# Optimization experiments

Hardware: AMD Instinct MI355X
Metric: run time of the kernel (lower is better)

The kernel has to match this reference:

```python
import jax, jax.numpy as jnp
import numpy as np

N, E = 50000, 800000
IN_DIM, HID, H, L = 256, 128, 4, 2
HD = HID // H
EPS = 1e-5


def _bn(x, g, b):
    # training-mode BatchNorm1d: biased variance over batch dim, eps=1e-5
    m = x.mean(0)
    v = jnp.var(x, axis=0)
    return g * (x - m) * jax.lax.rsqrt(v + EPS) + b


def _seg_softmax(scores, dst, n):
    # scores: [E, H]; softmax over edges sharing the same dst node
    m = jax.ops.segment_max(scores, dst, num_segments=n)  # [N, H]
    e = jnp.exp(scores - m[dst])
    s = jax.ops.segment_sum(e, dst, num_segments=n)
    return e / s[dst]


def _attn_layer(h, src, dst, wq, bq, wk, bk, wv, bv, wo, bo):
    n = h.shape[0]
    scale = 1.0 / np.sqrt(HD)
    Q = (h @ wq + bq).reshape(n, H, HD)
    K = (h @ wk + bk).reshape(n, H, HD)
    V = (h @ wv + bv).reshape(n, H, HD)
    # per-edge scores: Q of src dotted with K of dst
    scores = jnp.einsum('ehd,ehd->eh', Q[src], K[dst]) * scale  # [E, H]
    attn = _seg_softmax(scores, dst, n)                         # [E, H]
    # weighted scatter-sum of V gathered at dst (faithful to source)
    out = jax.ops.segment_sum(attn[:, :, None] * V[dst], dst, num_segments=n)
    out = out.reshape(n, HID) @ wo + bo
    return jax.nn.relu(out)


def setup_inputs() -> dict:
    key = jax.random.key(0)
    ks = jax.random.split(key, 20)
    s = 0.05  # weight scale to keep activations tame
    inp = {
        'x': jax.random.normal(ks[0], (N, IN_DIM), jnp.float32),
        'edge_index': jax.random.randint(ks[1], (2, E), 0, N),
        'W_enc1': jax.random.normal(ks[2], (IN_DIM, HID), jnp.float32) * s,
        'b_enc1': jax.random.normal(ks[3], (HID,), jnp.float32) * s,
        'g1': jnp.ones((HID,), jnp.float32),
        'beta1': jnp.zeros((HID,), jnp.float32),
        'W_enc2': jax.random.normal(ks[4], (HID, HID), jnp.float32) * s,
        'b_enc2': jax.random.normal(ks[5], (HID,), jnp.float32) * s,
        'g2': jnp.ones((HID,), jnp.float32),
        'beta2': jnp.zeros((HID,), jnp.float32),
        'Wq': jax.random.normal(ks[6], (L, HID, HID), jnp.float32) * s,
        'bq': jax.random.normal(ks[7], (L, HID), jnp.float32) * s,
        'Wk': jax.random.normal(ks[8], (L, HID, HID), jnp.float32) * s,
        'bk': jax.random.normal(ks[9], (L, HID), jnp.float32) * s,
        'Wv': jax.random.normal(ks[10], (L, HID, HID), jnp.float32) * s,
        'bv': jax.random.normal(ks[11], (L, HID), jnp.float32) * s,
        'Wo': jax.random.normal(ks[12], (L, HID, HID), jnp.float32) * s,
        'bo': jax.random.normal(ks[13], (L, HID), jnp.float32) * s,
    }
    return inp


def reference(x, edge_index, W_enc1, b_enc1, g1, beta1, W_enc2, b_enc2, g2, beta2,
              Wq, bq, Wk, bk, Wv, bv, Wo, bo):
    src, dst = edge_index[0], edge_index[1]
    # encoder: Linear -> BN -> ReLU -> (dropout=id) -> Linear -> BN -> ReLU
    h = jax.nn.relu(_bn(x @ W_enc1 + b_enc1, g1, beta1))
    h = jax.nn.relu(_bn(h @ W_enc2 + b_enc2, g2, beta2))
    for i in range(L):
        h = _attn_layer(h, src, dst, Wq[i], bq[i], Wk[i], bk[i],
                        Wv[i], bv[i], Wo[i], bo[i])
    return h
```

## Files before the change

kernel.cpp:

```cpp
#include <hip/hip_runtime.h>

#define NN 50000
#define NE 800000
#define NB 782
#define TOTF 114688

typedef unsigned short u16;
typedef unsigned int u32;
typedef __attribute__((ext_vector_type(8))) short s8v;
typedef __attribute__((ext_vector_type(4))) float f4v;

__device__ __forceinline__ void split2(float f, u16& h, u16& lo) {
    u32 u = __float_as_uint(f);
    h = (u16)(u >> 16);
    float r = f - __uint_as_float(u & 0xFFFF0000u);
    lo = (u16)(__float_as_uint(r) >> 16);
}

__global__ void mask_scatter_k(const int* __restrict__ dst, float* __restrict__ mask) {
    int i = blockIdx.x * blockDim.x + threadIdx.x;
    if (i < NE) mask[dst[i]] = 1.0f;
}

__global__ void prep_w_k(const float* __restrict__ W1, const float* __restrict__ W2,
                         const float* __restrict__ Wv, const float* __restrict__ Wo,
                         u16* __restrict__ fh, u16* __restrict__ fl) {
    int idx = blockIdx.x * 256 + threadIdx.x;
    if (idx >= TOTF) return;
    const float* W;
    int local;
    if (idx < 32768) { W = W1; local = idx; }
    else {
        int t = idx - 32768;
        int m = t >> 14;
        local = t & 16383;
        if (m == 0) W = W2;
        else if (m == 1) W = Wv;
        else if (m == 2) W = Wo;
        else if (m == 3) W = Wv + 16384;
        else W = Wo + 16384;
    }
    int j = local & 7, l = (local >> 3) & 63, nt = (local >> 9) & 7, kc = local >> 12;
    int k = kc * 32 + ((l >> 4) << 3) + j;
    int n = nt * 16 + (l & 15);
    u16 h, lo;
    split2(W[k * 128 + n], h, lo);
    fh[idx] = h;
    fl[idx] = lo;
}

__global__ __launch_bounds__(64)
void redstats_k(const float* __restrict__ pst, float* __restrict__ st) {
    int c = blockIdx.x;
    float s = 0.f;
    for (int b = threadIdx.x; b < NB; b += 64) s += pst[(size_t)b * 256 + c];
    s += __shfl_xor(s, 1);  s += __shfl_xor(s, 2);  s += __shfl_xor(s, 4);
    s += __shfl_xor(s, 8);  s += __shfl_xor(s, 16); s += __shfl_xor(s, 32);
    if (threadIdx.x == 0) st[c] = s;
}

template<int KC, int FOLD, int STATS>
__global__ __launch_bounds__(512, 6)
void mgemm_k(const float* __restrict__ A,
             const u16* __restrict__ fh, const u16* __restrict__ fl,
             const float* __restrict__ bias,
             const float* __restrict__ fst,
             const float* __restrict__ fg, const float* __restrict__ fbe,
             float* __restrict__ pst,
             float* __restrict__ C) {
    constexpr int KP = KC / 4;
    __shared__ __align__(16) u16 Ah[64][136];
    __shared__ __align__(16) u16 Al[64][136];
    __shared__ float scl[128], shf[128];
    const int tid = threadIdx.x;
    const int l = tid & 63, w = tid >> 6;
    const int q = l >> 4, cc = l & 15;
    const int sl = w >> 1, hf = w & 1;
    const int row0 = blockIdx.x * 64;

    if (FOLD && tid < 128) {
        float mean = fst[tid] * (1.0f / NN);
        float var = fst[128 + tid] * (1.0f / NN) - mean * mean;
        float rstd = rsqrtf(var + 1e-5f);
        float ga = fg[tid] * rstd;
        scl[tid] = ga;
        shf[tid] = fbe[tid] - mean * ga;
    }

    f4v zf = {0.f, 0.f, 0.f, 0.f};
    f4v acc[4];
#pragma unroll
    for (int t = 0; t < 4; ++t) acc[t] = zf;

    for (int p = 0; p < KP; ++p) {
        if (p > 0 || FOLD) __syncthreads();
#pragma unroll
        for (int it = 0; it < 4; ++it) {
            int lin = tid + 512 * it;
            int r = lin >> 5;
            int c4 = (lin & 31) * 4;
            int gr = row0 + r; if (gr > NN - 1) gr = NN - 1;
            float4 f = *(const float4*)(A + (size_t)gr * (KC * 32) + p * 128 + c4);
            float v[4] = {f.x, f.y, f.z, f.w};
            if (FOLD) {
#pragma unroll
                for (int m = 0; m < 4; ++m) {
                    float t = v[m] * scl[c4 + m] + shf[c4 + m];
                    v[m] = t > 0.f ? t : 0.f;
                }
            }
            ushort4 uh, ul;
            split2(v[0], uh.x, ul.x); split2(v[1], uh.y, ul.y);
            split2(v[2], uh.z, ul.z); split2(v[3], uh.w, ul.w);
            *(ushort4*)&Ah[r][c4] = uh;
            *(ushort4*)&Al[r][c4] = ul;
        }
        __syncthreads();
#pragma unroll
        for (int kc = 0; kc < 4; ++kc) {
            int kcg = p * 4 + kc;
            s8v ah = *(const s8v*)&Ah[16 * sl + cc][kc * 32 + q * 8];
            s8v al = *(const s8v*)&Al[16 * sl + cc][kc * 32 + q * 8];
#pragma unroll
            for (int t = 0; t < 4; ++t) {
                const int fo = kcg * 4096 + (4 * hf + t) * 512 + l * 8;
                s8v bh = *(const s8v*)(fh + fo);
                s8v bl = *(const s8v*)(fl + fo);
                acc[t] = __builtin_amdgcn_mfma_f32_16x16x32_bf16(ah, bh, acc[t], 0, 0, 0);
                acc[t] = __builtin_amdgcn_mfma_f32_16x16x32_bf16(ah, bl, acc[t], 0, 0, 0);
                acc[t] = __builtin_amdgcn_mfma_f32_16x16x32_bf16(al, bh, acc[t], 0, 0, 0);
            }
        }
    }

    float ps[4], pq[4];
#pragma unroll
    for (int t = 0; t < 4; ++t) { ps[t] = 0.f; pq[t] = 0.f; }
#pragma unroll
    for (int t = 0; t < 4; ++t) {
        int col = (4 * hf + t) * 16 + cc;
        float bb = bias[col];
#pragma unroll
        for (int r = 0; r < 4; ++r) {
            int gr = row0 + 16 * sl + q * 4 + r;
            float val = acc[t][r] + bb;
            if (gr < NN) {
                C[(size_t)gr * 128 + col] = val;
                if (STATS) { ps[t] += val; pq[t] += val * val; }
            }
        }
    }
    if (STATS) {
        __syncthreads();
        float* wredS = (float*)&Ah[0][0];
        float* wredQ = wredS + 512;
#pragma unroll
        for (int t = 0; t < 4; ++t) {
            ps[t] += __shfl_xor(ps[t], 16); ps[t] += __shfl_xor(ps[t], 32);
            pq[t] += __shfl_xor(pq[t], 16); pq[t] += __shfl_xor(pq[t], 32);
        }
        if (l < 16) {
#pragma unroll
            for (int t = 0; t < 4; ++t) {
                int col = (4 * hf + t) * 16 + l;
                wredS[sl * 128 + col] = ps[t];
                wredQ[sl * 128 + col] = pq[t];
            }
        }
        __syncthreads();
        if (tid < 256) {
            int c = tid & 127;
            const float* src = (tid < 128) ? wredS : wredQ;
            pst[(size_t)blockIdx.x * 256 + tid] =
                src[c] + src[128 + c] + src[256 + c] + src[384 + c];
        }
    }
}

__global__ __launch_bounds__(512, 6)
void mmega_k(const float* __restrict__ X,
             const u16* __restrict__ fh, const u16* __restrict__ fl,
             const float* __restrict__ bv, const float* __restrict__ bo,
             const float* __restrict__ fst,
             const float* __restrict__ fg, const float* __restrict__ fbe,
             const float* __restrict__ mask, float* __restrict__ out) {
    __shared__ __align__(16) u16 Ah[64][136];
    __shared__ __align__(16) u16 Al[64][136];
    __shared__ float scl[128], shf[128];
    const int tid = threadIdx.x;
    const int l = tid & 63, w = tid >> 6;
    const int q = l >> 4, cc = l & 15;
    const int sl = w >> 1, hf = w & 1;
    const int row0 = blockIdx.x * 64;

    if (tid < 128) {
        float mean = fst[tid] * (1.0f / NN);
        float var = fst[128 + tid] * (1.0f / NN) - mean * mean;
        float rstd = rsqrtf(var + 1e-5f);
        float ga = fg[tid] * rstd;
        scl[tid] = ga;
        shf[tid] = fbe[tid] - mean * ga;
    }
    __syncthreads();

    float rm[4];
#pragma unroll
    for (int r = 0; r < 4; ++r) {
        int gr = row0 + 16 * sl + q * 4 + r;
        rm[r] = (gr < NN) ? mask[gr] : 0.f;
    }

#pragma unroll
    for (int it = 0; it < 4; ++it) {
        int lin = tid + 512 * it;
        int r = lin >> 5;
        int c4 = (lin & 31) * 4;
        int gr = row0 + r; if (gr > NN - 1) gr = NN - 1;
        float4 f = *(const float4*)(X + (size_t)gr * 128 + c4);
        float v[4] = {f.x, f.y, f.z, f.w};
        ushort4 uh, ul;
#pragma unroll
        for (int m = 0; m < 4; ++m) {
            float t = v[m] * scl[c4 + m] + shf[c4 + m];
            v[m] = t > 0.f ? t : 0.f;
        }
        split2(v[0], uh.x, ul.x); split2(v[1], uh.y, ul.y);
        split2(v[2], uh.z, ul.z); split2(v[3], uh.w, ul.w);
        *(ushort4*)&Ah[r][c4] = uh;
        *(ushort4*)&Al[r][c4] = ul;
    }
    __syncthreads();

    f4v zf = {0.f, 0.f, 0.f, 0.f};
    for (int s = 0; s < 4; ++s) {
        const u16* WH = fh + s * 16384;
        const u16* WL = fl + s * 16384;
        const float* bp = (s == 0) ? bv : (s == 1) ? bo : (s == 2) ? (bv + 128) : (bo + 128);

        f4v acc[4];
#pragma unroll
        for (int t = 0; t < 4; ++t) acc[t] = zf;
#pragma unroll
        for (int kc = 0; kc < 4; ++kc) {
            s8v ah = *(const s8v*)&Ah[16 * sl + cc][kc * 32 + q * 8];
            s8v al = *(const s8v*)&Al[16 * sl + cc][kc * 32 + q * 8];
#pragma unroll
            for (int t = 0; t < 4; ++t) {
                const int fo = kc * 4096 + (4 * hf + t) * 512 + l * 8;
                s8v bh = *(const s8v*)(WH + fo);
                s8v bl = *(const s8v*)(WL + fo);
                acc[t] = __builtin_amdgcn_mfma_f32_16x16x32_bf16(ah, bh, acc[t], 0, 0, 0);
                acc[t] = __builtin_amdgcn_mfma_f32_16x16x32_bf16(ah, bl, acc[t], 0, 0, 0);
                acc[t] = __builtin_amdgcn_mfma_f32_16x16x32_bf16(al, bh, acc[t], 0, 0, 0);
            }
        }

        if (s == 3) {
#pragma unroll
            for (int t = 0; t < 4; ++t) {
                int col = (4 * hf + t) * 16 + cc;
                float bb = bp[col];
#pragma unroll
                for (int r = 0; r < 4; ++r) {
                    int gr = row0 + 16 * sl + q * 4 + r;
                    if (gr < NN)
                        out[(size_t)gr * 128 + col] = fmaxf(acc[t][r] + bb, 0.f);
                }
            }
        } else {
            __syncthreads();
#pragma unroll
            for (int t = 0; t < 4; ++t) {
                int col = (4 * hf + t) * 16 + cc;
                float bb = bp[col];
#pragma unroll
                for (int r = 0; r < 4; ++r) {
                    int rl = 16 * sl + q * 4 + r;
                    float val = acc[t][r] + bb;
                    val = (s == 1) ? fmaxf(val, 0.f) : val * rm[r];
                    u16 h, lo; split2(val, h, lo);
                    Ah[rl][col] = h;
                    Al[rl][col] = lo;
                }
            }
            __syncthreads();
        }
    }
}

extern "C" void kernel_launch(void* const* d_in, const int* in_sizes, int n_in,
                              void* d_out, int out_size, void* d_ws, size_t ws_size,
                              hipStream_t stream) {
    const float* x   = (const float*)d_in[0];
    const int*   ei  = (const int*)d_in[1];
    const float* W1  = (const float*)d_in[2];
    const float* b1  = (const float*)d_in[3];
    const float* g1  = (const float*)d_in[4];
    const float* be1 = (const float*)d_in[5];
    const float* W2  = (const float*)d_in[6];
    const float* b2  = (const float*)d_in[7];
    const float* g2  = (const float*)d_in[8];
    const float* be2 = (const float*)d_in[9];
    const float* Wv  = (const float*)d_in[14];
    const float* bv  = (const float*)d_in[15];
    const float* Wo  = (const float*)d_in[16];
    const float* bo  = (const float*)d_in[17];

    float* out = (float*)d_out;

    char* ws = (char*)d_ws;
    float* buf  = (float*)(ws);
    float* mask = (float*)(ws + 25600000);
    float* st1  = (float*)(ws + 25800704);
    float* st2  = st1 + 256;
    u16*   fH   = (u16*)(ws + 25804800);
    u16*   fL   = fH + TOTF;
    float* pst  = (float*)(ws + 26263552);

    hipMemsetAsync(mask, 0, NN * sizeof(float), stream);
    mask_scatter_k<<<dim3((NE + 255) / 256), dim3(256), 0, stream>>>(ei + NE, mask);
    prep_w_k<<<dim3((TOTF + 255) / 256), dim3(256), 0, stream>>>(W1, W2, Wv, Wo, fH, fL);

    dim3 gg(NB), bb(512);
    mgemm_k<8, 0, 1><<<gg, bb, 0, stream>>>(x, fH, fL, b1,
                                            nullptr, nullptr, nullptr, pst, buf);
    redstats_k<<<dim3(256), dim3(64), 0, stream>>>(pst, st1);
    mgemm_k<4, 1, 1><<<gg, bb, 0, stream>>>(buf, fH + 32768, fL + 32768, b2,
                                            st1, g1, be1, pst, out);
    redstats_k<<<dim3(256), dim3(64), 0, stream>>>(pst, st2);
    mmega_k<<<gg, bb, 0, stream>>>(out, fH + 49152, fL + 49152, bv, bo,
                                   st2, g2, be2, mask, out);
}
```

Baseline: 227.3 us.

## Give each wave a private 32-row by 128-column tile to drop block barriers

The GEMM kernels switch from 512-thread blocks over 64 rows to 256-thread blocks over 128 rows. Each wave now owns 32 full rows: it stages them into LDS, computes all eight column tiles with two row-tile accumulators, and in the chained mmega kernel writes its intermediate results back only to its own rows. Because no wave reads another wave's rows, most __syncthreads calls go away, and each weight fragment loaded from global memory feeds twice as many MFMAs. In exchange each thread holds more accumulator registers (launch bounds drop to 2 blocks per CU), the grid halves to 391 blocks, which can leave the CUs unevenly loaded, and every wave has to load its own rows with less parallelism per row.

```diff
diff --git a/kernel.cpp b/kernel.cpp
--- a/kernel.cpp
+++ b/kernel.cpp
@@ -2,7 +2,7 @@
 
 #define NN 50000
 #define NE 800000
-#define NB 782
+#define NB 391
 #define TOTF 114688
 
 typedef unsigned short u16;
@@ -60,7 +60,7 @@
 }
 
 template<int KC, int FOLD, int STATS>
-__global__ __launch_bounds__(512, 6)
+__global__ __launch_bounds__(256, 2)
 void mgemm_k(const float* __restrict__ A,
              const u16* __restrict__ fh, const u16* __restrict__ fl,
              const float* __restrict__ bias,
@@ -68,39 +68,41 @@
              const float* __restrict__ fg, const float* __restrict__ fbe,
              float* __restrict__ pst,
              float* __restrict__ C) {
+    constexpr int K = KC * 32;
     constexpr int KP = KC / 4;
-    __shared__ __align__(16) u16 Ah[64][136];
-    __shared__ __align__(16) u16 Al[64][136];
+    __shared__ __align__(16) u16 Ah[128][136];
+    __shared__ __align__(16) u16 Al[128][136];
     __shared__ float scl[128], shf[128];
     const int tid = threadIdx.x;
     const int l = tid & 63, w = tid >> 6;
     const int q = l >> 4, cc = l & 15;
-    const int sl = w >> 1, hf = w & 1;
-    const int row0 = blockIdx.x * 64;
-
-    if (FOLD && tid < 128) {
-        float mean = fst[tid] * (1.0f / NN);
-        float var = fst[128 + tid] * (1.0f / NN) - mean * mean;
-        float rstd = rsqrtf(var + 1e-5f);
-        float ga = fg[tid] * rstd;
-        scl[tid] = ga;
-        shf[tid] = fbe[tid] - mean * ga;
+    const int row0 = blockIdx.x * 128;
+
+    if (FOLD) {
+        if (tid < 128) {
+            float mean = fst[tid] * (1.0f / NN);
+            float var = fst[128 + tid] * (1.0f / NN) - mean * mean;
+            float rstd = rsqrtf(var + 1e-5f);
+            float ga = fg[tid] * rstd;
+            scl[tid] = ga;
+            shf[tid] = fbe[tid] - mean * ga;
+        }
+        __syncthreads();
     }
 
     f4v zf = {0.f, 0.f, 0.f, 0.f};
-    f4v acc[4];
-#pragma unroll
-    for (int t = 0; t < 4; ++t) acc[t] = zf;
+    f4v acc0[8], acc1[8];
+#pragma unroll
+    for (int nt = 0; nt < 8; ++nt) { acc0[nt] = zf; acc1[nt] = zf; }
 
     for (int p = 0; p < KP; ++p) {
-        if (p > 0 || FOLD) __syncthreads();
-#pragma unroll
-        for (int it = 0; it < 4; ++it) {
-            int lin = tid + 512 * it;
+#pragma unroll
+        for (int it = 0; it < 16; ++it) {
+            int lin = it * 64 + l;
             int r = lin >> 5;
             int c4 = (lin & 31) * 4;
-            int gr = row0 + r; if (gr > NN - 1) gr = NN - 1;
-            float4 f = *(const float4*)(A + (size_t)gr * (KC * 32) + p * 128 + c4);
+            int gr = row0 + 32 * w + r; if (gr > NN - 1) gr = NN - 1;
+            float4 f = *(const float4*)(A + (size_t)gr * K + p * 128 + c4);
             float v[4] = {f.x, f.y, f.z, f.w};
             if (FOLD) {
 #pragma unroll
@@ -112,41 +114,48 @@
             ushort4 uh, ul;
             split2(v[0], uh.x, ul.x); split2(v[1], uh.y, ul.y);
             split2(v[2], uh.z, ul.z); split2(v[3], uh.w, ul.w);
-            *(ushort4*)&Ah[r][c4] = uh;
-            *(ushort4*)&Al[r][c4] = ul;
-        }
-        __syncthreads();
+            *(ushort4*)&Ah[32 * w + r][c4] = uh;
+            *(ushort4*)&Al[32 * w + r][c4] = ul;
+        }
 #pragma unroll
         for (int kc = 0; kc < 4; ++kc) {
             int kcg = p * 4 + kc;
-            s8v ah = *(const s8v*)&Ah[16 * sl + cc][kc * 32 + q * 8];
-            s8v al = *(const s8v*)&Al[16 * sl + cc][kc * 32 + q * 8];
-#pragma unroll
-            for (int t = 0; t < 4; ++t) {
-                const int fo = kcg * 4096 + (4 * hf + t) * 512 + l * 8;
+            s8v ah0 = *(const s8v*)&Ah[32 * w + cc][kc * 32 + q * 8];
+            s8v al0 = *(const s8v*)&Al[32 * w + cc][kc * 32 + q * 8];
+            s8v ah1 = *(const s8v*)&Ah[32 * w + 16 + cc][kc * 32 + q * 8];
+            s8v al1 = *(const s8v*)&Al[32 * w + 16 + cc][kc * 32 + q * 8];
+#pragma unroll
+            for (int nt = 0; nt < 8; ++nt) {
+                const int fo = kcg * 4096 + nt * 512 + l * 8;
                 s8v bh = *(const s8v*)(fh + fo);
                 s8v bl = *(const s8v*)(fl + fo);
-                acc[t] = __builtin_amdgcn_mfma_f32_16x16x32_bf16(ah, bh, acc[t], 0, 0, 0);
-                acc[t] = __builtin_amdgcn_mfma_f32_16x16x32_bf16(ah, bl, acc[t], 0, 0, 0);
-                acc[t] = __builtin_amdgcn_mfma_f32_16x16x32_bf16(al, bh, acc[t], 0, 0, 0);
-            }
-        }
-    }
-
-    float ps[4], pq[4];
-#pragma unroll
-    for (int t = 0; t < 4; ++t) { ps[t] = 0.f; pq[t] = 0.f; }
-#pragma unroll
-    for (int t = 0; t < 4; ++t) {
-        int col = (4 * hf + t) * 16 + cc;
+                acc0[nt] = __builtin_amdgcn_mfma_f32_16x16x32_bf16(ah0, bh, acc0[nt], 0, 0, 0);
+                acc0[nt] = __builtin_amdgcn_mfma_f32_16x16x32_bf16(ah0, bl, acc0[nt], 0, 0, 0);
+                acc0[nt] = __builtin_amdgcn_mfma_f32_16x16x32_bf16(al0, bh, acc0[nt], 0, 0, 0);
+                acc1[nt] = __builtin_amdgcn_mfma_f32_16x16x32_bf16(ah1, bh, acc1[nt], 0, 0, 0);
+                acc1[nt] = __builtin_amdgcn_mfma_f32_16x16x32_bf16(ah1, bl, acc1[nt], 0, 0, 0);
+                acc1[nt] = __builtin_amdgcn_mfma_f32_16x16x32_bf16(al1, bh, acc1[nt], 0, 0, 0);
+            }
+        }
+    }
+
+    float ps[8], pq[8];
+#pragma unroll
+    for (int nt = 0; nt < 8; ++nt) { ps[nt] = 0.f; pq[nt] = 0.f; }
+#pragma unroll
+    for (int nt = 0; nt < 8; ++nt) {
+        int col = nt * 16 + cc;
         float bb = bias[col];
 #pragma unroll
-        for (int r = 0; r < 4; ++r) {
-            int gr = row0 + 16 * sl + q * 4 + r;
-            float val = acc[t][r] + bb;
-            if (gr < NN) {
-                C[(size_t)gr * 128 + col] = val;
-                if (STATS) { ps[t] += val; pq[t] += val * val; }
+        for (int rt = 0; rt < 2; ++rt) {
+#pragma unroll
+            for (int r = 0; r < 4; ++r) {
+                int gr = row0 + 32 * w + 16 * rt + q * 4 + r;
+                float val = (rt ? acc1[nt][r] : acc0[nt][r]) + bb;
+                if (gr < NN) {
+                    C[(size_t)gr * 128 + col] = val;
+                    if (STATS) { ps[nt] += val; pq[nt] += val * val; }
+                }
             }
         }
     }
@@ -155,20 +164,19 @@
         float* wredS = (float*)&Ah[0][0];
         float* wredQ = wredS + 512;
 #pragma unroll
-        for (int t = 0; t < 4; ++t) {
-            ps[t] += __shfl_xor(ps[t], 16); ps[t] += __shfl_xor(ps[t], 32);
-            pq[t] += __shfl_xor(pq[t], 16); pq[t] += __shfl_xor(pq[t], 32);
+        for (int nt = 0; nt < 8; ++nt) {
+            ps[nt] += __shfl_xor(ps[nt], 16); ps[nt] += __shfl_xor(ps[nt], 32);
+            pq[nt] += __shfl_xor(pq[nt], 16); pq[nt] += __shfl_xor(pq[nt], 32);
         }
         if (l < 16) {
 #pragma unroll
-            for (int t = 0; t < 4; ++t) {
-                int col = (4 * hf + t) * 16 + l;
-                wredS[sl * 128 + col] = ps[t];
-                wredQ[sl * 128 + col] = pq[t];
+            for (int nt = 0; nt < 8; ++nt) {
+                wredS[w * 128 + nt * 16 + l] = ps[nt];
+                wredQ[w * 128 + nt * 16 + l] = pq[nt];
             }
         }
         __syncthreads();
-        if (tid < 256) {
+        {
             int c = tid & 127;
             const float* src = (tid < 128) ? wredS : wredQ;
             pst[(size_t)blockIdx.x * 256 + tid] =
@@ -177,21 +185,20 @@
     }
 }
 
-__global__ __launch_bounds__(512, 6)
+__global__ __launch_bounds__(256, 2)
 void mmega_k(const float* __restrict__ X,
              const u16* __restrict__ fh, const u16* __restrict__ fl,
              const float* __restrict__ bv, const float* __restrict__ bo,
              const float* __restrict__ fst,
              const float* __restrict__ fg, const float* __restrict__ fbe,
              const float* __restrict__ mask, float* __restrict__ out) {
-    __shared__ __align__(16) u16 Ah[64][136];
-    __shared__ __align__(16) u16 Al[64][136];
+    __shared__ __align__(16) u16 Ah[128][136];
+    __shared__ __align__(16) u16 Al[128][136];
     __shared__ float scl[128], shf[128];
     const int tid = threadIdx.x;
     const int l = tid & 63, w = tid >> 6;
     const int q = l >> 4, cc = l & 15;
-    const int sl = w >> 1, hf = w & 1;
-    const int row0 = blockIdx.x * 64;
+    const int row0 = blockIdx.x * 128;
 
     if (tid < 128) {
         float mean = fst[tid] * (1.0f / NN);
@@ -203,33 +210,34 @@
     }
     __syncthreads();
 
-    float rm[4];
-#pragma unroll
-    for (int r = 0; r < 4; ++r) {
-        int gr = row0 + 16 * sl + q * 4 + r;
-        rm[r] = (gr < NN) ? mask[gr] : 0.f;
-    }
-
-#pragma unroll
-    for (int it = 0; it < 4; ++it) {
-        int lin = tid + 512 * it;
+    float rm[2][4];
+#pragma unroll
+    for (int rt = 0; rt < 2; ++rt)
+#pragma unroll
+        for (int r = 0; r < 4; ++r) {
+            int gr = row0 + 32 * w + 16 * rt + q * 4 + r;
+            rm[rt][r] = (gr < NN) ? mask[gr] : 0.f;
+        }
+
+#pragma unroll
+    for (int it = 0; it < 16; ++it) {
+        int lin = it * 64 + l;
         int r = lin >> 5;
         int c4 = (lin & 31) * 4;
-        int gr = row0 + r; if (gr > NN - 1) gr = NN - 1;
+        int gr = row0 + 32 * w + r; if (gr > NN - 1) gr = NN - 1;
         float4 f = *(const float4*)(X + (size_t)gr * 128 + c4);
         float v[4] = {f.x, f.y, f.z, f.w};
-        ushort4 uh, ul;
 #pragma unroll
         for (int m = 0; m < 4; ++m) {
             float t = v[m] * scl[c4 + m] + shf[c4 + m];
             v[m] = t > 0.f ? t : 0.f;
         }
+        ushort4 uh, ul;
         split2(v[0], uh.x, ul.x); split2(v[1], uh.y, ul.y);
         split2(v[2], uh.z, ul.z); split2(v[3], uh.w, ul.w);
-        *(ushort4*)&Ah[r][c4] = uh;
-        *(ushort4*)&Al[r][c4] = ul;
-    }
-    __syncthreads();
+        *(ushort4*)&Ah[32 * w + r][c4] = uh;
+        *(ushort4*)&Al[32 * w + r][c4] = ul;
+    }
 
     f4v zf = {0.f, 0.f, 0.f, 0.f};
     for (int s = 0; s < 4; ++s) {
@@ -237,53 +245,61 @@
         const u16* WL = fl + s * 16384;
         const float* bp = (s == 0) ? bv : (s == 1) ? bo : (s == 2) ? (bv + 128) : (bo + 128);
 
-        f4v acc[4];
-#pragma unroll
-        for (int t = 0; t < 4; ++t) acc[t] = zf;
+        f4v acc0[8], acc1[8];
+#pragma unroll
+        for (int nt = 0; nt < 8; ++nt) { acc0[nt] = zf; acc1[nt] = zf; }
 #pragma unroll
         for (int kc = 0; kc < 4; ++kc) {
-            s8v ah = *(const s8v*)&Ah[16 * sl + cc][kc * 32 + q * 8];
-            s8v al = *(const s8v*)&Al[16 * sl + cc][kc * 32 + q * 8];
-#pragma unroll
-            for (int t = 0; t < 4; ++t) {
-                const int fo = kc * 4096 + (4 * hf + t) * 512 + l * 8;
+            s8v ah0 = *(const s8v*)&Ah[32 * w + cc][kc * 32 + q * 8];
+            s8v al0 = *(const s8v*)&Al[32 * w + cc][kc * 32 + q * 8];
+            s8v ah1 = *(const s8v*)&Ah[32 * w + 16 + cc][kc * 32 + q * 8];
+            s8v al1 = *(const s8v*)&Al[32 * w + 16 + cc][kc * 32 + q * 8];
+#pragma unroll
+            for (int nt = 0; nt < 8; ++nt) {
+                const int fo = kc * 4096 + nt * 512 + l * 8;
                 s8v bh = *(const s8v*)(WH + fo);
                 s8v bl = *(const s8v*)(WL + fo);
-                acc[t] = __builtin_amdgcn_mfma_f32_16x16x32_bf16(ah, bh, acc[t], 0, 0, 0);
-                acc[t] = __builtin_amdgcn_mfma_f32_16x16x32_bf16(ah, bl, acc[t], 0, 0, 0);
-                acc[t] = __builtin_amdgcn_mfma_f32_16x16x32_bf16(al, bh, acc[t], 0, 0, 0);
+                acc0[nt] = __builtin_amdgcn_mfma_f32_16x16x32_bf16(ah0, bh, acc0[nt], 0, 0, 0);
+                acc0[nt] = __builtin_amdgcn_mfma_f32_16x16x32_bf16(ah0, bl, acc0[nt], 0, 0, 0);
+                acc0[nt] = __builtin_amdgcn_mfma_f32_16x16x32_bf16(al0, bh, acc0[nt], 0, 0, 0);
+                acc1[nt] = __builtin_amdgcn_mfma_f32_16x16x32_bf16(ah1, bh, acc1[nt], 0, 0, 0);
+                acc1[nt] = __builtin_amdgcn_mfma_f32_16x16x32_bf16(ah1, bl, acc1[nt], 0, 0, 0);
+                acc1[nt] = __builtin_amdgcn_mfma_f32_16x16x32_bf16(al1, bh, acc1[nt], 0, 0, 0);
             }
         }
 
         if (s == 3) {
 #pragma unroll
-            for (int t = 0; t < 4; ++t) {
-                int col = (4 * hf + t) * 16 + cc;
+            for (int nt = 0; nt < 8; ++nt) {
+                int col = nt * 16 + cc;
                 float bb = bp[col];
 #pragma unroll
-                for (int r = 0; r < 4; ++r) {
-                    int gr = row0 + 16 * sl + q * 4 + r;
-                    if (gr < NN)
-                        out[(size_t)gr * 128 + col] = fmaxf(acc[t][r] + bb, 0.f);
-                }
+                for (int rt = 0; rt < 2; ++rt)
+#pragma unroll
+                    for (int r = 0; r < 4; ++r) {
+                        int gr = row0 + 32 * w + 16 * rt + q * 4 + r;
+                        if (gr < NN)
+                            out[(size_t)gr * 128 + col] =
+                                fmaxf((rt ? acc1[nt][r] : acc0[nt][r]) + bb, 0.f);
+                    }
             }
         } else {
-            __syncthreads();
-#pragma unroll
-            for (int t = 0; t < 4; ++t) {
-                int col = (4 * hf + t) * 16 + cc;
+#pragma unroll
+            for (int nt = 0; nt < 8; ++nt) {
+                int col = nt * 16 + cc;
                 float bb = bp[col];
 #pragma unroll
-                for (int r = 0; r < 4; ++r) {
-                    int rl = 16 * sl + q * 4 + r;
-                    float val = acc[t][r] + bb;
-                    val = (s == 1) ? fmaxf(val, 0.f) : val * rm[r];
-                    u16 h, lo; split2(val, h, lo);
-                    Ah[rl][col] = h;
-                    Al[rl][col] = lo;
-                }
-            }
-            __syncthreads();
+                for (int rt = 0; rt < 2; ++rt)
+#pragma unroll
+                    for (int r = 0; r < 4; ++r) {
+                        int rl = 32 * w + 16 * rt + q * 4 + r;
+                        float val = (rt ? acc1[nt][r] : acc0[nt][r]) + bb;
+                        val = (s == 1) ? fmaxf(val, 0.f) : val * rm[rt][r];
+                        u16 h, lo; split2(val, h, lo);
+                        Ah[rl][col] = h;
+                        Al[rl][col] = lo;
+                    }
+            }
         }
     }
 }
@@ -321,7 +337,7 @@
     mask_scatter_k<<<dim3((NE + 255) / 256), dim3(256), 0, stream>>>(ei + NE, mask);
     prep_w_k<<<dim3((TOTF + 255) / 256), dim3(256), 0, stream>>>(W1, W2, Wv, Wo, fH, fL);
 
-    dim3 gg(NB), bb(512);
+    dim3 gg(NB), bb(256);
     mgemm_k<8, 0, 1><<<gg, bb, 0, stream>>>(x, fH, fL, b1,
                                             nullptr, nullptr, nullptr, pst, buf);
     redstats_k<<<dim3(256), dim3(64), 0, stream>>>(pst, st1);
```

Measured after the change: 239.6 us. 1.05x slower.
